# Optimization experiments

Hardware: AMD Instinct MI355X
Metric: run time of the kernel (lower is better)

The kernel has to match this reference:

```python
import jax, jax.numpy as jnp
import numpy as np

# Production-scale dims
B, C, T = 4, 4096, 2048      # batch, river nodes, timesteps
BS = 16                      # block_size
K = 100                      # max_delay (IRF taps)
NNZ = 1024                   # nonzero 16x16 blocks in river-network kernel
NB = C // BS                 # number of node blocks
DT = 1.0                     # dt


def setup_inputs() -> dict:
    key = jax.random.key(0)
    k1, k2, k3, k4 = jax.random.split(key, 4)
    runoff = jax.random.normal(k1, (B, C, T), jnp.float32)
    # per-entry IRF parameters (storage constants), in [0,1) -> tau in [1,20)
    params = jax.random.uniform(k2, (NNZ, BS, BS), jnp.float32)
    block_rows = jax.random.randint(k3, (NNZ,), 0, NB, jnp.int32)
    block_cols = jax.random.randint(k4, (NNZ,), 0, NB, jnp.int32)
    return {"runoff": runoff, "params": params,
            "block_rows": block_rows, "block_cols": block_cols}


def _build_kernel(params):
    # linear_storage IRF (discrete linear reservoir, cascade=1):
    #   a = exp(-dt/tau),  h[k] = (1 - a) * a**k,  k = 0..K-1 (sums ~ 1)
    tau = 1.0 + 19.0 * params                      # [NNZ, BS, BS]
    a = jnp.exp(-DT / tau)
    ks = jnp.arange(K, dtype=jnp.float32)
    h = (1.0 - a)[..., None] * jnp.power(a[..., None], ks)  # [NNZ,BS,BS,K]
    return h


def _route(runoff, params, block_rows, block_cols):
    h = _build_kernel(params)                      # [NNZ, BS(out), BS(in), K]
    # lax.conv is cross-correlation; flip taps for causal y[t]=sum_k h[k] x[t-k]
    w = h[..., ::-1].reshape(NNZ * BS, BS, K)      # grouped-conv rhs (OIH)
    xb = runoff.reshape(B, NB, BS, T)
    xg = jnp.take(xb, block_cols, axis=1)          # gather source blocks [B,NNZ,BS,T]
    xg = xg.reshape(B, NNZ * BS, T)
    # block-sparse causal conv == grouped 1D conv with left padding K-1
    y = jax.lax.conv_general_dilated(
        xg, w, window_strides=(1,), padding=[(K - 1, 0)],
        feature_group_count=NNZ, dimension_numbers=("NCH", "OIH", "NCH"))
    y = y.reshape(B, NNZ, BS, T).transpose(1, 0, 2, 3)   # [NNZ,B,BS,T]
    y = jax.ops.segment_sum(y, block_rows, num_segments=NB)  # scatter-add rows
    y = y.transpose(1, 0, 2, 3).reshape(B, C, T)
    # g.include_index_diag is False -> identity added explicitly
    return runoff + y


def reference(runoff, params, block_rows, block_cols):
    return _route(runoff, params, block_rows, block_cols)
```

## Files before the change

kernel.cpp:

```cpp
#include <hip/hip_runtime.h>

#define BB 4
#define CC 4096
#define TT 2048
#define BS 16
#define KK 100
#define NNZ 1024
#define NB (CC / BS)
#define MAXM 64
#define TC 256
#define NCH (TT / TC)
#define SSTR 260
#define HSTR 108

#define WS_CNT   0u
#define WS_PERM  1024u
#define WS_LIST  2048u
#define WS_S0    1048576u
#define S0_BYTES ((size_t)NNZ * BB * NCH * 256 * 4)
#define WS_NEED  ((size_t)WS_S0 + S0_BYTES)

template <int CTRL>
__device__ __forceinline__ float add_dpp(float acc, float src) {
    int m = __builtin_amdgcn_update_dpp(0, __builtin_bit_cast(int, src),
                                        CTRL, 0xF, 0xF, true);
    return acc + __builtin_bit_cast(float, m);
}
__device__ __forceinline__ float add_xor4(float keep, float send) {
    int m = __builtin_amdgcn_ds_swizzle(__builtin_bit_cast(int, send), 0x101F);
    return keep + __builtin_bit_cast(float, m);
}

__device__ __forceinline__ float butterfly16(const float (&v)[16], int j) {
    const bool q0 = (j & 1) != 0;
    const bool q1 = (j & 2) != 0;
    const bool q2 = (j & 4) != 0;
    const bool q3 = (j & 8) != 0;
    float u[8];
#pragma unroll
    for (int p = 0; p < 8; ++p) {
        float keep = q0 ? v[2 * p + 1] : v[2 * p];
        float send = q0 ? v[2 * p]     : v[2 * p + 1];
        u[p] = add_dpp<0xB1>(keep, send);
    }
    float w[4];
#pragma unroll
    for (int p = 0; p < 4; ++p) {
        float keep = q1 ? u[2 * p + 1] : u[2 * p];
        float send = q1 ? u[2 * p]     : u[2 * p + 1];
        w[p] = add_dpp<0x4E>(keep, send);
    }
    float z[2];
#pragma unroll
    for (int p = 0; p < 2; ++p) {
        float keep = q3 ? w[p + 2] : w[p];
        float send = q3 ? w[p]     : w[p + 2];
        z[p] = add_dpp<0x128>(keep, send);
    }
    float keep = q2 ? z[1] : z[0];
    float send = q2 ? z[0] : z[1];
    return add_xor4(keep, send);
}

__global__ __launch_bounds__(64) void lti_build_lists(
    const int* __restrict__ rows, int* __restrict__ cnt,
    int* __restrict__ list) {
    const int r = blockIdx.x;
    const int lane = threadIdx.x;
    int m = 0;
    for (int base = 0; base < NNZ; base += 64) {
        const int n = base + lane;
        const bool hit = (rows[n] == r);
        const unsigned long long mask = __ballot(hit);
        if (hit) {
            const int pos =
                m + __popcll(mask & ((1ull << lane) - 1ull));
            if (pos < MAXM) list[r * MAXM + pos] = n;
        }
        m += (int)__popcll(mask);
    }
    if (lane == 0) cnt[r] = (m < MAXM) ? m : MAXM;
}

__global__ void lti_rank(const int* __restrict__ cnt, int* __restrict__ perm) {
    __shared__ int sc[NB];
    const int r = threadIdx.x;
    sc[r] = cnt[r];
    __syncthreads();
    const int my = sc[r];
    int rank = 0;
    for (int q = 0; q < NB; ++q) {
        int cq = sc[q];
        if (cq > my || (cq == my && q < r)) ++rank;
    }
    perm[rank] = r;
}

__global__ __launch_bounds__(256) void lti_bootstrap(
    const float* __restrict__ x, const float* __restrict__ params,
    const int* __restrict__ cols, float* __restrict__ s0)
{
    const int n  = blockIdx.x;
    const int b  = blockIdx.y;
    const int ch = blockIdx.z + 1;
    const int tid = threadIdx.x;
    const int j = tid & 15;

    __shared__ __align__(16) float hx[16 * HSTR];

    const float* __restrict__ xw =
        x + ((size_t)b * CC + (size_t)cols[n] * BS) * TT + ch * TC - KK;
    {
        const int f0 = tid;
        const int row0 = f0 / 25, q0 = f0 - row0 * 25;
        if (f0 < 400) {
            *(float4*)&hx[row0 * HSTR + 4 * q0] =
                *(const float4*)(xw + (size_t)row0 * TT + 4 * q0);
        }
        const int f1 = tid + 256;
        const int row1 = f1 / 25, q1 = f1 - row1 * 25;
        if (f1 < 400) {
            *(float4*)&hx[row1 * HSTR + 4 * q1] =
                *(const float4*)(xw + (size_t)row1 * TT + 4 * q1);
        }
    }
    __syncthreads();

    const float pv  = params[n * (BS * BS) + tid];
    const float tau = 1.0f + 19.0f * pv;
    const float a   = __expf(-1.0f / tau);

    const float* __restrict__ hj = &hx[j * HSTR];
    float s = 0.0f;
#pragma unroll 5
    for (int q = 0; q < 25; ++q) {
        float4 h = *(const float4*)(hj + 4 * q);
        s = fmaf(a, s, h.x); s = fmaf(a, s, h.y);
        s = fmaf(a, s, h.z); s = fmaf(a, s, h.w);
    }
    s0[((size_t)(n * BB + b) * NCH + ch) * 256 + tid] = s;
}

__global__ __launch_bounds__(256) void lti_router(
    const float* __restrict__ x,
    const float* __restrict__ params,
    const int* __restrict__ cols,
    const int* __restrict__ cnt,
    const int* __restrict__ list,
    const int* __restrict__ perm,
    const float* __restrict__ s0,
    float* __restrict__ out)
{
    const int r   = perm[blockIdx.x];
    const int b   = blockIdx.y;
    const int ch  = blockIdx.z;
    const int t0  = ch * TC;
    const int tid = threadIdx.x;
    const int j    = tid & 15;
    const int i    = tid >> 4;
    const int lane = tid & 63;
    const int wv   = tid >> 6;

    __shared__ __align__(16) float xs[4][16 * SSTR];

    float acc[16];
#pragma unroll
    for (int p = 0; p < 16; ++p) acc[p] = 0.0f;

    const int m = cnt[r];
    const int pairs = (m + 1) >> 1;
    const size_t xbase = (size_t)b * CC * TT;

    float aA = 0.f, oA = 0.f, aB = 0.f, oB = 0.f, s0A = 0.f, s0B = 0.f;
    if (m > 0) {
        const int nA = list[r * MAXM + 0];
        const bool vB = (m > 1);
        const int nB = vB ? list[r * MAXM + 1] : nA;
        const float pvA = params[nA * (BS * BS) + tid];
        const float pvB = params[nB * (BS * BS) + tid];
        s0A = (ch == 0) ? 0.0f
            : s0[((size_t)(nA * BB + b) * NCH + ch) * 256 + tid];
        s0B = (ch == 0 || !vB) ? 0.0f
            : s0[((size_t)(nB * BB + b) * NCH + ch) * 256 + tid];
        const float* __restrict__ xA = x + xbase + (size_t)cols[nA] * BS * TT;
        const float* __restrict__ xB = x + xbase + (size_t)cols[nB] * BS * TT;
#pragma unroll
        for (int k = 0; k < 4; ++k) {
            const int row = wv + 4 * k;
            *(float4*)&xs[0][row * SSTR + lane * 4] =
                *(const float4*)(xA + (size_t)row * TT + t0 + lane * 4);
            *(float4*)&xs[1][row * SSTR + lane * 4] =
                *(const float4*)(xB + (size_t)row * TT + t0 + lane * 4);
        }
        aA = __expf(-1.0f / (1.0f + 19.0f * pvA));
        oA = 1.0f - aA;
        const float aBt = __expf(-1.0f / (1.0f + 19.0f * pvB));
        aB = vB ? aBt : 0.0f;
        oB = vB ? (1.0f - aBt) : 0.0f;
    }
    __syncthreads();

    int cur = 0;
    for (int pi = 0; pi < pairs; ++pi) {
        const bool has = (pi + 1 < pairs);
        float pvNA = 0.f, pvNB = 0.f, s0NA = 0.f, s0NB = 0.f;
        bool vNB = false;
        float4 XA0, XA1, XA2, XA3, XB0, XB1, XB2, XB3;
        if (has) {
            const int ia = 2 * (pi + 1);
            const int nA = list[r * MAXM + ia];
            vNB = (ia + 1 < m);
            const int nB = vNB ? list[r * MAXM + ia + 1] : nA;
            pvNA = params[nA * (BS * BS) + tid];
            pvNB = params[nB * (BS * BS) + tid];
            s0NA = (ch == 0) ? 0.0f
                 : s0[((size_t)(nA * BB + b) * NCH + ch) * 256 + tid];
            s0NB = (ch == 0 || !vNB) ? 0.0f
                 : s0[((size_t)(nB * BB + b) * NCH + ch) * 256 + tid];
            const float* __restrict__ xA =
                x + xbase + (size_t)cols[nA] * BS * TT;
            const float* __restrict__ xB =
                x + xbase + (size_t)cols[nB] * BS * TT;
            XA0 = *(const float4*)(xA + (size_t)(wv +  0) * TT + t0 + lane * 4);
            XA1 = *(const float4*)(xA + (size_t)(wv +  4) * TT + t0 + lane * 4);
            XA2 = *(const float4*)(xA + (size_t)(wv +  8) * TT + t0 + lane * 4);
            XA3 = *(const float4*)(xA + (size_t)(wv + 12) * TT + t0 + lane * 4);
            XB0 = *(const float4*)(xB + (size_t)(wv +  0) * TT + t0 + lane * 4);
            XB1 = *(const float4*)(xB + (size_t)(wv +  4) * TT + t0 + lane * 4);
            XB2 = *(const float4*)(xB + (size_t)(wv +  8) * TT + t0 + lane * 4);
            XB3 = *(const float4*)(xB + (size_t)(wv + 12) * TT + t0 + lane * 4);
        }

        const float* __restrict__ xjA = &xs[2 * cur][j * SSTR];
        const float* __restrict__ xjB = &xs[2 * cur + 1][j * SSTR];
        float sA = s0A, sB = s0B;
#pragma unroll
        for (int tb = 0; tb < 16; ++tb) {
            float4 A0 = *(const float4*)(xjA + tb * 16 + 0);
            float4 A1 = *(const float4*)(xjA + tb * 16 + 4);
            float4 A2 = *(const float4*)(xjA + tb * 16 + 8);
            float4 A3 = *(const float4*)(xjA + tb * 16 + 12);
            float4 B0 = *(const float4*)(xjB + tb * 16 + 0);
            float4 B1 = *(const float4*)(xjB + tb * 16 + 4);
            float4 B2 = *(const float4*)(xjB + tb * 16 + 8);
            float4 B3 = *(const float4*)(xjB + tb * 16 + 12);
            float va[16], vb[16];
            va[0]=A0.x;  va[1]=A0.y;  va[2]=A0.z;  va[3]=A0.w;
            va[4]=A1.x;  va[5]=A1.y;  va[6]=A1.z;  va[7]=A1.w;
            va[8]=A2.x;  va[9]=A2.y;  va[10]=A2.z; va[11]=A2.w;
            va[12]=A3.x; va[13]=A3.y; va[14]=A3.z; va[15]=A3.w;
            vb[0]=B0.x;  vb[1]=B0.y;  vb[2]=B0.z;  vb[3]=B0.w;
            vb[4]=B1.x;  vb[5]=B1.y;  vb[6]=B1.z;  vb[7]=B1.w;
            vb[8]=B2.x;  vb[9]=B2.y;  vb[10]=B2.z; vb[11]=B2.w;
            vb[12]=B3.x; vb[13]=B3.y; vb[14]=B3.z; vb[15]=B3.w;

            float v[16];
#pragma unroll
            for (int t = 0; t < 16; ++t) {
                sA = fmaf(aA, sA, va[t]);
                sB = fmaf(aB, sB, vb[t]);
                v[t] = fmaf(oB, sB, oA * sA);
            }
            acc[tb] += butterfly16(v, j);
        }

        if (has) {
            const int nxt = cur ^ 1;
            float* __restrict__ dA = &xs[2 * nxt][0];
            float* __restrict__ dB = &xs[2 * nxt + 1][0];
            *(float4*)&dA[(wv +  0) * SSTR + lane * 4] = XA0;
            *(float4*)&dA[(wv +  4) * SSTR + lane * 4] = XA1;
            *(float4*)&dA[(wv +  8) * SSTR + lane * 4] = XA2;
            *(float4*)&dA[(wv + 12) * SSTR + lane * 4] = XA3;
            *(float4*)&dB[(wv +  0) * SSTR + lane * 4] = XB0;
            *(float4*)&dB[(wv +  4) * SSTR + lane * 4] = XB1;
            *(float4*)&dB[(wv +  8) * SSTR + lane * 4] = XB2;
            *(float4*)&dB[(wv + 12) * SSTR + lane * 4] = XB3;
            aA = __expf(-1.0f / (1.0f + 19.0f * pvNA));
            oA = 1.0f - aA;
            const float aBt = __expf(-1.0f / (1.0f + 19.0f * pvNB));
            aB = vNB ? aBt : 0.0f;
            oB = vNB ? (1.0f - aBt) : 0.0f;
            s0A = s0NA; s0B = s0NB;
            cur = nxt;
        }
        __syncthreads();
    }

    const size_t obase = ((size_t)b * CC + (size_t)r * BS + i) * TT + t0;
#pragma unroll
    for (int p = 0; p < 16; ++p) {
        const int t = p * 16 + j;
        out[obase + t] = x[obase + t] + acc[p];
    }
}

#define FTC 256
#define FNCH (TT / FTC)
#define FWPAD 128
#define FSSTR 388

__global__ __launch_bounds__(256) void lti_router_fb(
    const float* __restrict__ x, const float* __restrict__ params,
    const int* __restrict__ cols, const int* __restrict__ cnt,
    const int* __restrict__ list, float* __restrict__ out)
{
    const int r   = blockIdx.x;
    const int b   = blockIdx.y;
    const int t0  = blockIdx.z * FTC;
    const int tid = threadIdx.x;
    const int j   = tid & 15;
    const int i   = tid >> 4;

    __shared__ __align__(16) float xs[16 * FSSTR];

    float acc[16];
#pragma unroll
    for (int p = 0; p < 16; ++p) acc[p] = 0.0f;

    const int m = cnt[r];
    for (int bi = 0; bi < m; ++bi) {
        const int n = list[r * MAXM + bi];
        const int c = cols[n];
        const float* __restrict__ xb =
            x + ((size_t)b * CC + (size_t)c * BS) * TT;
#pragma unroll
        for (int k = 0; k < 6; ++k) {
            const int f    = tid + k * 256;
            const int row  = f / 96;
            const int col4 = f - row * 96;
            const int t    = t0 - FWPAD + col4 * 4;
            float4 v;
            if (t >= 0) v = *(const float4*)(xb + (size_t)row * TT + t);
            else        v = make_float4(0.f, 0.f, 0.f, 0.f);
            *(float4*)&xs[row * FSSTR + col4 * 4] = v;
        }
        __syncthreads();

        const float pv  = params[n * (BS * BS) + tid];
        const float tau = 1.0f + 19.0f * pv;
        const float av  = __expf(-1.0f / tau);
        const float oma = 1.0f - av;

        const float* __restrict__ xj = &xs[j * FSSTR];
        float s = 0.0f;
        if (t0 != 0) {
#pragma unroll 5
            for (int q = 0; q < 25; ++q) {
                float4 h = *(const float4*)(xj + 28 + 4 * q);
                s = fmaf(av, s, h.x); s = fmaf(av, s, h.y);
                s = fmaf(av, s, h.z); s = fmaf(av, s, h.w);
            }
        }
        const float* __restrict__ xm = xj + FWPAD;
#pragma unroll
        for (int tb = 0; tb < 16; ++tb) {
            float4 V0 = *(const float4*)(xm + tb * 16 + 0);
            float4 V1 = *(const float4*)(xm + tb * 16 + 4);
            float4 V2 = *(const float4*)(xm + tb * 16 + 8);
            float4 V3 = *(const float4*)(xm + tb * 16 + 12);
            float v[16];
            v[0]=V0.x;  v[1]=V0.y;  v[2]=V0.z;  v[3]=V0.w;
            v[4]=V1.x;  v[5]=V1.y;  v[6]=V1.z;  v[7]=V1.w;
            v[8]=V2.x;  v[9]=V2.y;  v[10]=V2.z; v[11]=V2.w;
            v[12]=V3.x; v[13]=V3.y; v[14]=V3.z; v[15]=V3.w;
#pragma unroll
            for (int t = 0; t < 16; ++t) { s = fmaf(av, s, v[t]); v[t] = oma * s; }
            acc[tb] += butterfly16(v, j);
        }
        __syncthreads();
    }

    const size_t obase = ((size_t)b * CC + (size_t)r * BS + i) * TT + t0;
#pragma unroll
    for (int p = 0; p < 16; ++p) {
        const int t = p * 16 + j;
        out[obase + t] = x[obase + t] + acc[p];
    }
}

extern "C" void kernel_launch(void* const* d_in, const int* in_sizes, int n_in,
                              void* d_out, int out_size, void* d_ws, size_t ws_size,
                              hipStream_t stream) {
    const float* runoff = (const float*)d_in[0];
    const float* params = (const float*)d_in[1];
    const int* rows = (const int*)d_in[2];
    const int* cols = (const int*)d_in[3];
    float* out = (float*)d_out;

    if (ws_size >= WS_NEED) {
        int*   cnt  = (int*)((char*)d_ws + WS_CNT);
        int*   perm = (int*)((char*)d_ws + WS_PERM);
        int*   list = (int*)((char*)d_ws + WS_LIST);
        float* s0   = (float*)((char*)d_ws + WS_S0);

        lti_build_lists<<<NB, 64, 0, stream>>>(rows, cnt, list);
        lti_rank<<<1, 256, 0, stream>>>(cnt, perm);
        dim3 bgrid(NNZ, BB, NCH - 1);
        lti_bootstrap<<<bgrid, 256, 0, stream>>>(runoff, params, cols, s0);
        dim3 rgrid(NB, BB, NCH);
        lti_router<<<rgrid, 256, 0, stream>>>(runoff, params, cols, cnt,
                                              list, perm, s0, out);
    } else {
        int* cnt  = (int*)d_ws;
        int* list = (int*)((char*)d_ws + 1024);
        lti_build_lists<<<NB, 64, 0, stream>>>(rows, cnt, list);
        dim3 grid(NB, BB, FNCH);
        lti_router_fb<<<grid, 256, 0, stream>>>(runoff, params, cols, cnt,
                                                list, out);
    }
}
```

Measured before the change: 331.9 us.

## Split router thread work into two half-chunks, each covering two output rows

Each router thread now handles one half (128 steps) of the 256-step time chunk and two output rows (i and i+8). Previously each thread ran the full 256-step serial recurrence for a single row. The bootstrap kernel now computes initial states at 128-step granularity, which doubles its grid and the s0 buffer. The aim is to shorten the serial dependency chain per thread and reuse each shared-memory input load across two rows. The cost is more bootstrap work, more registers, and more s0 traffic.

```diff
diff --git a/kernel.cpp b/kernel.cpp
--- a/kernel.cpp
+++ b/kernel.cpp
@@ -10,6 +10,7 @@
 #define MAXM 64
 #define TC 256
 #define NCH (TT / TC)
+#define NHB (2 * NCH)
 #define SSTR 260
 #define HSTR 108
 
@@ -17,7 +18,7 @@
 #define WS_PERM  1024u
 #define WS_LIST  2048u
 #define WS_S0    1048576u
-#define S0_BYTES ((size_t)NNZ * BB * NCH * 256 * 4)
+#define S0_BYTES ((size_t)NNZ * BB * NHB * 256 * 4)
 #define WS_NEED  ((size_t)WS_S0 + S0_BYTES)
 
 template <int CTRL>
@@ -73,8 +74,7 @@
         const bool hit = (rows[n] == r);
         const unsigned long long mask = __ballot(hit);
         if (hit) {
-            const int pos =
-                m + __popcll(mask & ((1ull << lane) - 1ull));
+            const int pos = m + __popcll(mask & ((1ull << lane) - 1ull));
             if (pos < MAXM) list[r * MAXM + pos] = n;
         }
         m += (int)__popcll(mask);
@@ -102,14 +102,14 @@
 {
     const int n  = blockIdx.x;
     const int b  = blockIdx.y;
-    const int ch = blockIdx.z + 1;
+    const int hb = blockIdx.z + 1;
     const int tid = threadIdx.x;
     const int j = tid & 15;
 
     __shared__ __align__(16) float hx[16 * HSTR];
 
     const float* __restrict__ xw =
-        x + ((size_t)b * CC + (size_t)cols[n] * BS) * TT + ch * TC - KK;
+        x + ((size_t)b * CC + (size_t)cols[n] * BS) * TT + hb * 128 - KK;
     {
         const int f0 = tid;
         const int row0 = f0 / 25, q0 = f0 - row0 * 25;
@@ -138,7 +138,7 @@
         s = fmaf(a, s, h.x); s = fmaf(a, s, h.y);
         s = fmaf(a, s, h.z); s = fmaf(a, s, h.w);
     }
-    s0[((size_t)(n * BB + b) * NCH + ch) * 256 + tid] = s;
+    s0[((size_t)(n * BB + b) * NHB + hb) * 256 + tid] = s;
 }
 
 __global__ __launch_bounds__(256) void lti_router(
@@ -157,31 +157,49 @@
     const int t0  = ch * TC;
     const int tid = threadIdx.x;
     const int j    = tid & 15;
-    const int i    = tid >> 4;
+    const int ig   = (tid >> 4) & 7;
+    const int h    = tid >> 7;
     const int lane = tid & 63;
     const int wv   = tid >> 6;
+    const int hb   = ch * 2 + h;
+    const int sslot = tid & 127;
 
     __shared__ __align__(16) float xs[4][16 * SSTR];
 
-    float acc[16];
-#pragma unroll
-    for (int p = 0; p < 16; ++p) acc[p] = 0.0f;
+    float acc[2][8];
+#pragma unroll
+    for (int k = 0; k < 2; ++k)
+#pragma unroll
+        for (int p = 0; p < 8; ++p) acc[k][p] = 0.0f;
 
     const int m = cnt[r];
     const int pairs = (m + 1) >> 1;
     const size_t xbase = (size_t)b * CC * TT;
 
-    float aA = 0.f, oA = 0.f, aB = 0.f, oB = 0.f, s0A = 0.f, s0B = 0.f;
+    float aA[2], oA[2], aB[2], oB[2], s0A[2], s0B[2];
+#pragma unroll
+    for (int k = 0; k < 2; ++k) {
+        aA[k] = oA[k] = aB[k] = oB[k] = s0A[k] = s0B[k] = 0.0f;
+    }
     if (m > 0) {
         const int nA = list[r * MAXM + 0];
         const bool vB = (m > 1);
         const int nB = vB ? list[r * MAXM + 1] : nA;
-        const float pvA = params[nA * (BS * BS) + tid];
-        const float pvB = params[nB * (BS * BS) + tid];
-        s0A = (ch == 0) ? 0.0f
-            : s0[((size_t)(nA * BB + b) * NCH + ch) * 256 + tid];
-        s0B = (ch == 0 || !vB) ? 0.0f
-            : s0[((size_t)(nB * BB + b) * NCH + ch) * 256 + tid];
+#pragma unroll
+        for (int k = 0; k < 2; ++k) {
+            const int sl = sslot + 128 * k;
+            const float pvA = params[nA * (BS * BS) + sl];
+            const float pvB = params[nB * (BS * BS) + sl];
+            s0A[k] = (hb == 0) ? 0.0f
+                : s0[((size_t)(nA * BB + b) * NHB + hb) * 256 + sl];
+            s0B[k] = (hb == 0 || !vB) ? 0.0f
+                : s0[((size_t)(nB * BB + b) * NHB + hb) * 256 + sl];
+            aA[k] = __expf(-1.0f / (1.0f + 19.0f * pvA));
+            oA[k] = 1.0f - aA[k];
+            const float aBt = __expf(-1.0f / (1.0f + 19.0f * pvB));
+            aB[k] = vB ? aBt : 0.0f;
+            oB[k] = vB ? (1.0f - aBt) : 0.0f;
+        }
         const float* __restrict__ xA = x + xbase + (size_t)cols[nA] * BS * TT;
         const float* __restrict__ xB = x + xbase + (size_t)cols[nB] * BS * TT;
 #pragma unroll
@@ -192,18 +210,14 @@
             *(float4*)&xs[1][row * SSTR + lane * 4] =
                 *(const float4*)(xB + (size_t)row * TT + t0 + lane * 4);
         }
-        aA = __expf(-1.0f / (1.0f + 19.0f * pvA));
-        oA = 1.0f - aA;
-        const float aBt = __expf(-1.0f / (1.0f + 19.0f * pvB));
-        aB = vB ? aBt : 0.0f;
-        oB = vB ? (1.0f - aBt) : 0.0f;
     }
     __syncthreads();
 
     int cur = 0;
     for (int pi = 0; pi < pairs; ++pi) {
         const bool has = (pi + 1 < pairs);
-        float pvNA = 0.f, pvNB = 0.f, s0NA = 0.f, s0NB = 0.f;
+        float pvNA[2] = {0.f, 0.f}, pvNB[2] = {0.f, 0.f};
+        float s0NA[2] = {0.f, 0.f}, s0NB[2] = {0.f, 0.f};
         bool vNB = false;
         float4 XA0, XA1, XA2, XA3, XB0, XB1, XB2, XB3;
         if (has) {
@@ -211,12 +225,16 @@
             const int nA = list[r * MAXM + ia];
             vNB = (ia + 1 < m);
             const int nB = vNB ? list[r * MAXM + ia + 1] : nA;
-            pvNA = params[nA * (BS * BS) + tid];
-            pvNB = params[nB * (BS * BS) + tid];
-            s0NA = (ch == 0) ? 0.0f
-                 : s0[((size_t)(nA * BB + b) * NCH + ch) * 256 + tid];
-            s0NB = (ch == 0 || !vNB) ? 0.0f
-                 : s0[((size_t)(nB * BB + b) * NCH + ch) * 256 + tid];
+#pragma unroll
+            for (int k = 0; k < 2; ++k) {
+                const int sl = sslot + 128 * k;
+                pvNA[k] = params[nA * (BS * BS) + sl];
+                pvNB[k] = params[nB * (BS * BS) + sl];
+                s0NA[k] = (hb == 0) ? 0.0f
+                    : s0[((size_t)(nA * BB + b) * NHB + hb) * 256 + sl];
+                s0NB[k] = (hb == 0 || !vNB) ? 0.0f
+                    : s0[((size_t)(nB * BB + b) * NHB + hb) * 256 + sl];
+            }
             const float* __restrict__ xA =
                 x + xbase + (size_t)cols[nA] * BS * TT;
             const float* __restrict__ xB =
@@ -231,11 +249,11 @@
             XB3 = *(const float4*)(xB + (size_t)(wv + 12) * TT + t0 + lane * 4);
         }
 
-        const float* __restrict__ xjA = &xs[2 * cur][j * SSTR];
-        const float* __restrict__ xjB = &xs[2 * cur + 1][j * SSTR];
-        float sA = s0A, sB = s0B;
-#pragma unroll
-        for (int tb = 0; tb < 16; ++tb) {
+        const float* __restrict__ xjA = &xs[2 * cur][j * SSTR + h * 128];
+        const float* __restrict__ xjB = &xs[2 * cur + 1][j * SSTR + h * 128];
+        float sA0 = s0A[0], sB0 = s0B[0], sA1 = s0A[1], sB1 = s0B[1];
+#pragma unroll
+        for (int tb = 0; tb < 8; ++tb) {
             float4 A0 = *(const float4*)(xjA + tb * 16 + 0);
             float4 A1 = *(const float4*)(xjA + tb * 16 + 4);
             float4 A2 = *(const float4*)(xjA + tb * 16 + 8);
@@ -257,11 +275,18 @@
             float v[16];
 #pragma unroll
             for (int t = 0; t < 16; ++t) {
-                sA = fmaf(aA, sA, va[t]);
-                sB = fmaf(aB, sB, vb[t]);
-                v[t] = fmaf(oB, sB, oA * sA);
+                sA0 = fmaf(aA[0], sA0, va[t]);
+                sB0 = fmaf(aB[0], sB0, vb[t]);
+                v[t] = fmaf(oB[0], sB0, oA[0] * sA0);
             }
-            acc[tb] += butterfly16(v, j);
+            acc[0][tb] += butterfly16(v, j);
+#pragma unroll
+            for (int t = 0; t < 16; ++t) {
+                sA1 = fmaf(aA[1], sA1, va[t]);
+                sB1 = fmaf(aB[1], sB1, vb[t]);
+                v[t] = fmaf(oB[1], sB1, oA[1] * sA1);
+            }
+            acc[1][tb] += butterfly16(v, j);
         }
 
         if (has) {
@@ -276,22 +301,30 @@
             *(float4*)&dB[(wv +  4) * SSTR + lane * 4] = XB1;
             *(float4*)&dB[(wv +  8) * SSTR + lane * 4] = XB2;
             *(float4*)&dB[(wv + 12) * SSTR + lane * 4] = XB3;
-            aA = __expf(-1.0f / (1.0f + 19.0f * pvNA));
-            oA = 1.0f - aA;
-            const float aBt = __expf(-1.0f / (1.0f + 19.0f * pvNB));
-            aB = vNB ? aBt : 0.0f;
-            oB = vNB ? (1.0f - aBt) : 0.0f;
-            s0A = s0NA; s0B = s0NB;
+#pragma unroll
+            for (int k = 0; k < 2; ++k) {
+                aA[k] = __expf(-1.0f / (1.0f + 19.0f * pvNA[k]));
+                oA[k] = 1.0f - aA[k];
+                const float aBt = __expf(-1.0f / (1.0f + 19.0f * pvNB[k]));
+                aB[k] = vNB ? aBt : 0.0f;
+                oB[k] = vNB ? (1.0f - aBt) : 0.0f;
+                s0A[k] = s0NA[k]; s0B[k] = s0NB[k];
+            }
             cur = nxt;
         }
         __syncthreads();
     }
 
-    const size_t obase = ((size_t)b * CC + (size_t)r * BS + i) * TT + t0;
-#pragma unroll
-    for (int p = 0; p < 16; ++p) {
-        const int t = p * 16 + j;
-        out[obase + t] = x[obase + t] + acc[p];
+#pragma unroll
+    for (int k = 0; k < 2; ++k) {
+        const size_t obase =
+            ((size_t)b * CC + (size_t)r * BS + (ig + 8 * k)) * TT
+            + t0 + h * 128;
+#pragma unroll
+        for (int p = 0; p < 8; ++p) {
+            const size_t idx = obase + p * 16 + j;
+            out[idx] = x[idx] + acc[k][p];
+        }
     }
 }
 
@@ -396,7 +429,7 @@
 
         lti_build_lists<<<NB, 64, 0, stream>>>(rows, cnt, list);
         lti_rank<<<1, 256, 0, stream>>>(cnt, perm);
-        dim3 bgrid(NNZ, BB, NCH - 1);
+        dim3 bgrid(NNZ, BB, NHB - 1);
         lti_bootstrap<<<bgrid, 256, 0, stream>>>(runoff, params, cols, s0);
         dim3 rgrid(NB, BB, NCH);
         lti_router<<<rgrid, 256, 0, stream>>>(runoff, params, cols, cnt,
```

New measurement: 493.3 us. 1.49x slower.
